# Kernel tuning notes

Measured on AMD Instinct MI355X. Metric: run time of the kernel, lower is better.

## Reference

```python
import jax, jax.numpy as jnp
import numpy as np

N_NODES = 50000
N_EDGES = 800000
D_IN = 128
D_HID = 128
D_OUT = 128


def _graph_conv(x, src, dst, ew, w_rel, w_root, b):
    # PyG GraphConv: out_i = (sum_{j->i} ew_ji * x_j) @ w_rel.T + b + x_i @ w_root.T
    msg = x[src] * ew[:, None]                                   # [E, F] gather + scale
    agg = jax.ops.segment_sum(msg, dst, num_segments=x.shape[0])  # [N, F] scatter-add
    return agg @ w_rel.T + x @ w_root.T + b


def setup_inputs() -> dict:
    key = jax.random.key(0)
    ks = jax.random.split(key, 12)
    s = 0.05
    x = jax.random.normal(ks[0], (N_NODES, D_IN), dtype=jnp.float32)
    edge_index = jax.random.randint(ks[1], (2, N_EDGES), 0, N_NODES, dtype=jnp.int32)
    edge_weight = jax.random.uniform(ks[2], (N_EDGES,), dtype=jnp.float32)
    return {
        "x": x,
        "edge_index": edge_index,
        "edge_weight": edge_weight,
        "w1_rel": jax.random.normal(ks[3], (D_HID, D_IN), dtype=jnp.float32) * s,
        "w1_root": jax.random.normal(ks[4], (D_HID, D_IN), dtype=jnp.float32) * s,
        "b1": jnp.zeros((D_HID,), dtype=jnp.float32),
        "w2_rel": jax.random.normal(ks[5], (D_HID, D_HID), dtype=jnp.float32) * s,
        "w2_root": jax.random.normal(ks[6], (D_HID, D_HID), dtype=jnp.float32) * s,
        "b2": jnp.zeros((D_HID,), dtype=jnp.float32),
        "w3_rel": jax.random.normal(ks[7], (D_OUT, D_HID), dtype=jnp.float32) * s,
        "w3_root": jax.random.normal(ks[8], (D_OUT, D_HID), dtype=jnp.float32) * s,
        "b3": jnp.zeros((D_OUT,), dtype=jnp.float32),
    }


def reference(x, edge_index, edge_weight,
              w1_rel, w1_root, b1,
              w2_rel, w2_root, b2,
              w3_rel, w3_root, b3):
    src, dst = edge_index[0], edge_index[1]
    h = _graph_conv(x, src, dst, edge_weight, w1_rel, w1_root, b1)
    h = jax.nn.relu(h)  # dropout is identity in eval mode
    h = _graph_conv(h, src, dst, edge_weight, w2_rel, w2_root, b2)
    h = jax.nn.relu(h)
    out = _graph_conv(h, src, dst, edge_weight, w3_rel, w3_root, b3)
    return out
```

## Files before the change

### kernel.cpp

```cpp
#include <hip/hip_runtime.h>
#include <hip/hip_bf16.h>

#define DFEAT   128
#define BCAP    2048
#define NB_MAX  1024

typedef __attribute__((ext_vector_type(8))) short bf16x8;
typedef __attribute__((ext_vector_type(4))) float f32x4;
typedef unsigned int uint;


__global__ void cursor_init(int* __restrict__ cursor, int NB) {
    int b = blockIdx.x * 256 + threadIdx.x;
    if (b < NB) cursor[b] = b * BCAP;
}


__global__ __launch_bounds__(1024) void bin_scatter(const int* __restrict__ src,
                                                    const int* __restrict__ dst,
                                                    const float* __restrict__ ew,
                                                    int* __restrict__ cursor,
                                                    int2* __restrict__ bedges,
                                                    int E, int NB) {
    __shared__ int hist[NB_MAX];
    __shared__ int base[NB_MAX];
    const int tid = threadIdx.x;
    for (int b = tid; b < NB; b += 1024) hist[b] = 0;
    __syncthreads();

    int  s[8]; float w[8]; int bk[8]; int dl[8];
    const int i0 = blockIdx.x * 8192 + tid;
    #pragma unroll
    for (int k = 0; k < 8; ++k) {
        int i = i0 + k * 1024;
        if (i < E) {
            s[k] = src[i]; w[k] = ew[i];
            int d = dst[i];
            bk[k] = d >> 6; dl[k] = d & 63;
            atomicAdd(&hist[bk[k]], 1);
        } else bk[k] = -1;
    }
    __syncthreads();
    for (int b = tid; b < NB; b += 1024) {
        int c = hist[b];
        base[b] = (c > 0) ? atomicAdd(&cursor[b], c) : 0;
        hist[b] = 0;
    }
    __syncthreads();
    #pragma unroll
    for (int k = 0; k < 8; ++k) {
        if (bk[k] >= 0) {
            int r = atomicAdd(&hist[bk[k]], 1);
            int pos = base[bk[k]] + r;
            if (pos < ((bk[k] + 1) << 11)) {
                bedges[pos] = make_int2(s[k] | (dl[k] << 26), __float_as_int(w[k]));
            }
        }
    }
}


__global__ __launch_bounds__(1024) void bucket_sort(const int* __restrict__ cursor,
                                                    int2* __restrict__ bedges,
                                                    int* __restrict__ rowptr,
                                                    int* __restrict__ rowend, int N) {
    __shared__ int2 buf[BCAP];
    __shared__ int hist[64], pref[64], rank[64];
    const int b = blockIdx.x, tid = threadIdx.x;
    const int base = b << 11;
    const int cnt = cursor[b] - base;

    if (tid < 64) hist[tid] = 0;
    __syncthreads();
    for (int i = tid; i < cnt; i += 1024) {
        int2 e = bedges[base + i];
        buf[i] = e;
        atomicAdd(&hist[((uint)e.x) >> 26], 1);
    }
    __syncthreads();
    if (tid < 64) {
        int v = hist[tid];
        int s = v;
        #pragma unroll
        for (int off = 1; off < 64; off <<= 1) {
            int t = __shfl_up(s, off, 64);
            if (tid >= off) s += t;
        }
        pref[tid] = s - v;
        rank[tid] = 0;
        int node = b * 64 + tid;
        if (node < N) {
            rowptr[node] = base + (s - v);
            rowend[node] = base + s;
        }
    }
    __syncthreads();
    for (int i = tid; i < cnt; i += 1024) {
        int2 e = buf[i];
        int dl = ((uint)e.x) >> 26;
        int r = atomicAdd(&rank[dl], 1);
        bedges[base + pref[dl] + r] = e;
    }
}


__device__ __forceinline__ uint pack_bf16x2(float a, float b) {
    __hip_bfloat16 ba = __float2bfloat16(a);
    __hip_bfloat16 bb = __float2bfloat16(b);
    unsigned short ua = *(unsigned short*)&ba;
    unsigned short ub = *(unsigned short*)&bb;
    return (uint)ua | ((uint)ub << 16);
}

__global__ void cvt_kernel(const float* __restrict__ in, uint* __restrict__ out, int n2) {
    int i = blockIdx.x * 256 + threadIdx.x;
    if (i < n2) {
        float2 v = ((const float2*)in)[i];
        out[i] = pack_bf16x2(v.x, v.y);
    }
}


__global__ void prep_Bpack(const float* __restrict__ wrel, const float* __restrict__ wroot,
                           __hip_bfloat16* __restrict__ Bp) {
    int idx = blockIdx.x * 256 + threadIdx.x;
    if (idx >= 32768) return;
    int j     = idx & 7;
    int lane  = (idx >> 3) & 63;
    int nfrag = (idx >> 9) & 7;
    int kstep = idx >> 12;
    int k = kstep * 32 + (lane >> 4) * 8 + j;
    int n = nfrag * 16 + (lane & 15);
    float v = (k < 128) ? wrel[n * 128 + k] : wroot[n * 128 + (k - 128)];
    Bp[idx] = __float2bfloat16(v);
}


__global__ __launch_bounds__(256) void aggregate_bf16(const uint* __restrict__ f,
                                                      const int* __restrict__ rowptr,
                                                      const int* __restrict__ rowend,
                                                      const int2* __restrict__ bedges,
                                                      uint* __restrict__ aggB, int N) {
    const int wid = threadIdx.x >> 6, lane = threadIdx.x & 63;
    const int node = blockIdx.x * 4 + wid;
    if (node >= N) return;
    const int beg = rowptr[node];
    const int deg = rowend[node] - beg;
    const int grp = lane >> 4;
    const int sub = lane & 15;

    const uint4* f4 = (const uint4*)f;

    float acc[8];
    #pragma unroll
    for (int i = 0; i < 8; ++i) acc[i] = 0.f;

    int done = 0;
    while (done < deg) {
        const int chunk = min(deg - done, 64);
        int2 e = bedges[beg + done + min(lane, chunk - 1)];
        const int vsrc = e.x & 0x03FFFFFF;
        const int vwb  = (lane < chunk) ? e.y : 0;
        const int iters = (chunk + 7) & ~7;
        for (int j = 0; j < iters; j += 8) {
            const int   s0 = __shfl(vsrc, j + grp, 64);
            const float w0 = __int_as_float(__shfl(vwb, j + grp, 64));
            const int   s1 = __shfl(vsrc, j + 4 + grp, 64);
            const float w1 = __int_as_float(__shfl(vwb, j + 4 + grp, 64));
            const uint4 q0 = f4[(size_t)s0 * 16 + sub];
            const uint4 q1 = f4[(size_t)s1 * 16 + sub];
            acc[0] = fmaf(w0, __uint_as_float(q0.x << 16),          acc[0]);
            acc[1] = fmaf(w0, __uint_as_float(q0.x & 0xffff0000u),  acc[1]);
            acc[2] = fmaf(w0, __uint_as_float(q0.y << 16),          acc[2]);
            acc[3] = fmaf(w0, __uint_as_float(q0.y & 0xffff0000u),  acc[3]);
            acc[4] = fmaf(w0, __uint_as_float(q0.z << 16),          acc[4]);
            acc[5] = fmaf(w0, __uint_as_float(q0.z & 0xffff0000u),  acc[5]);
            acc[6] = fmaf(w0, __uint_as_float(q0.w << 16),          acc[6]);
            acc[7] = fmaf(w0, __uint_as_float(q0.w & 0xffff0000u),  acc[7]);
            acc[0] = fmaf(w1, __uint_as_float(q1.x << 16),          acc[0]);
            acc[1] = fmaf(w1, __uint_as_float(q1.x & 0xffff0000u),  acc[1]);
            acc[2] = fmaf(w1, __uint_as_float(q1.y << 16),          acc[2]);
            acc[3] = fmaf(w1, __uint_as_float(q1.y & 0xffff0000u),  acc[3]);
            acc[4] = fmaf(w1, __uint_as_float(q1.z << 16),          acc[4]);
            acc[5] = fmaf(w1, __uint_as_float(q1.z & 0xffff0000u),  acc[5]);
            acc[6] = fmaf(w1, __uint_as_float(q1.w << 16),          acc[6]);
            acc[7] = fmaf(w1, __uint_as_float(q1.w & 0xffff0000u),  acc[7]);
        }
        done += chunk;
    }

    #pragma unroll
    for (int i = 0; i < 8; ++i) {
        acc[i] += __shfl_xor(acc[i], 16, 64);
        acc[i] += __shfl_xor(acc[i], 32, 64);
    }

    if (lane < 16) {
        uint4 o;
        o.x = pack_bf16x2(acc[0], acc[1]);
        o.y = pack_bf16x2(acc[2], acc[3]);
        o.z = pack_bf16x2(acc[4], acc[5]);
        o.w = pack_bf16x2(acc[6], acc[7]);
        ((uint4*)aggB)[(size_t)node * 16 + sub] = o;
    }
}


template<int RELU, int OUTF32>
__global__ __launch_bounds__(256) void gemm_mfma(const uint* __restrict__ Aagg,
                                                 const uint* __restrict__ f,
                                                 const bf16x8* __restrict__ Bp,
                                                 const float* __restrict__ bias,
                                                 float* __restrict__ outf,
                                                 __hip_bfloat16* __restrict__ outb, int M) {
    const int tid  = threadIdx.x;
    const int lane = tid & 63, wid = tid >> 6;
    const int wr = wid >> 1, wc = wid & 1;
    const int m0 = blockIdx.x * 128 + wr * 64;
    const int n0 = wc * 64;

    f32x4 acc[4][4];
    #pragma unroll
    for (int mi = 0; mi < 4; ++mi)
        #pragma unroll
        for (int ni = 0; ni < 4; ++ni) acc[mi][ni] = (f32x4){0.f, 0.f, 0.f, 0.f};

    const short* Aa = (const short*)Aagg;
    const short* Ar = (const short*)f;
    const int lrow = lane & 15;
    const int lk   = (lane >> 4) * 8;
    int rowidx[4];
    #pragma unroll
    for (int mi = 0; mi < 4; ++mi) {
        int r = m0 + mi * 16 + lrow;
        rowidx[mi] = (r < M) ? r : (M - 1);
    }

    #pragma unroll
    for (int ks = 0; ks < 8; ++ks) {
        const short* Abase = (ks < 4) ? Aa : Ar;
        const int koff = (ks & 3) * 32 + lk;
        bf16x8 a[4], b[4];
        #pragma unroll
        for (int mi = 0; mi < 4; ++mi)
            a[mi] = *(const bf16x8*)(Abase + (size_t)rowidx[mi] * 128 + koff);
        #pragma unroll
        for (int ni = 0; ni < 4; ++ni)
            b[ni] = Bp[(ks * 8 + (wc * 4 + ni)) * 64 + lane];
        #pragma unroll
        for (int mi = 0; mi < 4; ++mi)
            #pragma unroll
            for (int ni = 0; ni < 4; ++ni)
                acc[mi][ni] = __builtin_amdgcn_mfma_f32_16x16x32_bf16(a[mi], b[ni], acc[mi][ni], 0, 0, 0);
    }

    const int crow = (lane >> 4) * 4;
    const int ccol = lane & 15;
    #pragma unroll
    for (int mi = 0; mi < 4; ++mi) {
        #pragma unroll
        for (int ni = 0; ni < 4; ++ni) {
            int col = n0 + ni * 16 + ccol;
            float bv = bias[col];
            #pragma unroll
            for (int r = 0; r < 4; ++r) {
                int row = m0 + mi * 16 + crow + r;
                if (row < M) {
                    float v = acc[mi][ni][r] + bv;
                    if (RELU) v = fmaxf(v, 0.f);
                    if (OUTF32) outf[(size_t)row * 128 + col] = v;
                    else        outb[(size_t)row * 128 + col] = __float2bfloat16(v);
                }
            }
        }
    }
}


extern "C" void kernel_launch(void* const* d_in, const int* in_sizes, int n_in,
                              void* d_out, int out_size, void* d_ws, size_t ws_size,
                              hipStream_t stream) {
    const float* x   = (const float*)d_in[0];
    const int*  eidx = (const int*)d_in[1];
    const float* ew  = (const float*)d_in[2];
    const float* w1r = (const float*)d_in[3];
    const float* w1t = (const float*)d_in[4];
    const float* b1  = (const float*)d_in[5];
    const float* w2r = (const float*)d_in[6];
    const float* w2t = (const float*)d_in[7];
    const float* b2  = (const float*)d_in[8];
    const float* w3r = (const float*)d_in[9];
    const float* w3t = (const float*)d_in[10];
    const float* b3  = (const float*)d_in[11];
    float* out = (float*)d_out;

    const int N  = in_sizes[0] / DFEAT;
    const int E  = in_sizes[2];
    const int NB = (N + 63) / 64;

    char* ws = (char*)d_ws;
    size_t off = 0;
    auto alloc = [&](size_t bytes) -> void* {
        off = (off + 255) & ~(size_t)255;
        void* p = ws + off;
        off += bytes;
        return p;
    };
    int*  cursor = (int*)alloc((size_t)NB * 4);
    int*  rowptr = (int*)alloc((size_t)N * 4);
    int*  rowend = (int*)alloc((size_t)N * 4);
    int2* bedges = (int2*)alloc((size_t)NB * BCAP * 8);
    __hip_bfloat16* Bp1 = (__hip_bfloat16*)alloc(32768 * 2);
    __hip_bfloat16* Bp2 = (__hip_bfloat16*)alloc(32768 * 2);
    __hip_bfloat16* Bp3 = (__hip_bfloat16*)alloc(32768 * 2);
    uint* xb   = (uint*)alloc((size_t)N * 64 * 4);
    uint* aggB = (uint*)alloc((size_t)N * 64 * 4);
    uint* h1b  = (uint*)alloc((size_t)N * 64 * 4);
    uint* h2b  = (uint*)alloc((size_t)N * 64 * 4);
    (void)ws_size;

    const int* src = eidx;
    const int* dst = eidx + E;

    cursor_init<<<(NB + 255) / 256, 256, 0, stream>>>(cursor, NB);
    bin_scatter<<<(E + 8191) / 8192, 1024, 0, stream>>>(src, dst, ew, cursor, bedges, E, NB);
    bucket_sort<<<NB, 1024, 0, stream>>>(cursor, bedges, rowptr, rowend, N);

    cvt_kernel<<<(N * 64 + 255) / 256, 256, 0, stream>>>(x, xb, N * 64);
    prep_Bpack<<<128, 256, 0, stream>>>(w1r, w1t, Bp1);
    prep_Bpack<<<128, 256, 0, stream>>>(w2r, w2t, Bp2);
    prep_Bpack<<<128, 256, 0, stream>>>(w3r, w3t, Bp3);

    const int aggGrid  = (N + 3) / 4;
    const int gemmGrid = (N + 127) / 128;

    aggregate_bf16<<<aggGrid, 256, 0, stream>>>(xb, rowptr, rowend, bedges, aggB, N);
    gemm_mfma<1, 0><<<gemmGrid, 256, 0, stream>>>(aggB, xb, (const bf16x8*)Bp1,
                                                  b1, nullptr, (__hip_bfloat16*)h1b, N);
    aggregate_bf16<<<aggGrid, 256, 0, stream>>>(h1b, rowptr, rowend, bedges, aggB, N);
    gemm_mfma<1, 0><<<gemmGrid, 256, 0, stream>>>(aggB, h1b, (const bf16x8*)Bp2,
                                                  b2, nullptr, (__hip_bfloat16*)h2b, N);
    aggregate_bf16<<<aggGrid, 256, 0, stream>>>(h2b, rowptr, rowend, bedges, aggB, N);
    gemm_mfma<0, 1><<<gemmGrid, 256, 0, stream>>>(aggB, h2b, (const bf16x8*)Bp3,
                                                  b3, out, nullptr, N);
}
```

Before: 178.3 us.

## Fuse aggregation into MFMA GEMM per 64-node tile and merge prep kernels

Each layer now runs one kernel: a 64-node tile block first aggregates neighbor features into a padded LDS tile (each wave handles 16 nodes sequentially), then runs the MFMA GEMM reading the aggregated half from LDS and the root half from global. This removes the aggB round trip through global memory and three kernel launches. Separately, the bf16 conversion, the weight packing and the cursor init are merged into one launch. The fused kernel uses a smaller grid (64 nodes per block, each wave serially walking 16 nodes), which may reduce latency hiding for the gather compared with one node per wave.

```diff
diff --git a/kernel.cpp b/kernel.cpp
--- a/kernel.cpp
+++ b/kernel.cpp
@@ -8,12 +8,6 @@
 typedef __attribute__((ext_vector_type(8))) short bf16x8;
 typedef __attribute__((ext_vector_type(4))) float f32x4;
 typedef unsigned int uint;
-
-
-__global__ void cursor_init(int* __restrict__ cursor, int NB) {
-    int b = blockIdx.x * 256 + threadIdx.x;
-    if (b < NB) cursor[b] = b * BCAP;
-}
 
 
 __global__ __launch_bounds__(1024) void bin_scatter(const int* __restrict__ src,
@@ -112,161 +106,178 @@
     return (uint)ua | ((uint)ub << 16);
 }
 
-__global__ void cvt_kernel(const float* __restrict__ in, uint* __restrict__ out, int n2) {
-    int i = blockIdx.x * 256 + threadIdx.x;
-    if (i < n2) {
-        float2 v = ((const float2*)in)[i];
-        out[i] = pack_bf16x2(v.x, v.y);
-    }
-}
-
-
-__global__ void prep_Bpack(const float* __restrict__ wrel, const float* __restrict__ wroot,
-                           __hip_bfloat16* __restrict__ Bp) {
-    int idx = blockIdx.x * 256 + threadIdx.x;
-    if (idx >= 32768) return;
-    int j     = idx & 7;
-    int lane  = (idx >> 3) & 63;
-    int nfrag = (idx >> 9) & 7;
-    int kstep = idx >> 12;
-    int k = kstep * 32 + (lane >> 4) * 8 + j;
-    int n = nfrag * 16 + (lane & 15);
-    float v = (k < 128) ? wrel[n * 128 + k] : wroot[n * 128 + (k - 128)];
-    Bp[idx] = __float2bfloat16(v);
-}
-
-
-__global__ __launch_bounds__(256) void aggregate_bf16(const uint* __restrict__ f,
-                                                      const int* __restrict__ rowptr,
-                                                      const int* __restrict__ rowend,
-                                                      const int2* __restrict__ bedges,
-                                                      uint* __restrict__ aggB, int N) {
-    const int wid = threadIdx.x >> 6, lane = threadIdx.x & 63;
-    const int node = blockIdx.x * 4 + wid;
-    if (node >= N) return;
-    const int beg = rowptr[node];
-    const int deg = rowend[node] - beg;
-    const int grp = lane >> 4;
-    const int sub = lane & 15;
-
-    const uint4* f4 = (const uint4*)f;
-
-    float acc[8];
-    #pragma unroll
-    for (int i = 0; i < 8; ++i) acc[i] = 0.f;
-
-    int done = 0;
-    while (done < deg) {
-        const int chunk = min(deg - done, 64);
-        int2 e = bedges[beg + done + min(lane, chunk - 1)];
-        const int vsrc = e.x & 0x03FFFFFF;
-        const int vwb  = (lane < chunk) ? e.y : 0;
-        const int iters = (chunk + 7) & ~7;
-        for (int j = 0; j < iters; j += 8) {
-            const int   s0 = __shfl(vsrc, j + grp, 64);
-            const float w0 = __int_as_float(__shfl(vwb, j + grp, 64));
-            const int   s1 = __shfl(vsrc, j + 4 + grp, 64);
-            const float w1 = __int_as_float(__shfl(vwb, j + 4 + grp, 64));
-            const uint4 q0 = f4[(size_t)s0 * 16 + sub];
-            const uint4 q1 = f4[(size_t)s1 * 16 + sub];
-            acc[0] = fmaf(w0, __uint_as_float(q0.x << 16),          acc[0]);
-            acc[1] = fmaf(w0, __uint_as_float(q0.x & 0xffff0000u),  acc[1]);
-            acc[2] = fmaf(w0, __uint_as_float(q0.y << 16),          acc[2]);
-            acc[3] = fmaf(w0, __uint_as_float(q0.y & 0xffff0000u),  acc[3]);
-            acc[4] = fmaf(w0, __uint_as_float(q0.z << 16),          acc[4]);
-            acc[5] = fmaf(w0, __uint_as_float(q0.z & 0xffff0000u),  acc[5]);
-            acc[6] = fmaf(w0, __uint_as_float(q0.w << 16),          acc[6]);
-            acc[7] = fmaf(w0, __uint_as_float(q0.w & 0xffff0000u),  acc[7]);
-            acc[0] = fmaf(w1, __uint_as_float(q1.x << 16),          acc[0]);
-            acc[1] = fmaf(w1, __uint_as_float(q1.x & 0xffff0000u),  acc[1]);
-            acc[2] = fmaf(w1, __uint_as_float(q1.y << 16),          acc[2]);
-            acc[3] = fmaf(w1, __uint_as_float(q1.y & 0xffff0000u),  acc[3]);
-            acc[4] = fmaf(w1, __uint_as_float(q1.z << 16),          acc[4]);
-            acc[5] = fmaf(w1, __uint_as_float(q1.z & 0xffff0000u),  acc[5]);
-            acc[6] = fmaf(w1, __uint_as_float(q1.w << 16),          acc[6]);
-            acc[7] = fmaf(w1, __uint_as_float(q1.w & 0xffff0000u),  acc[7]);
-        }
-        done += chunk;
-    }
-
-    #pragma unroll
-    for (int i = 0; i < 8; ++i) {
-        acc[i] += __shfl_xor(acc[i], 16, 64);
-        acc[i] += __shfl_xor(acc[i], 32, 64);
-    }
-
-    if (lane < 16) {
-        uint4 o;
-        o.x = pack_bf16x2(acc[0], acc[1]);
-        o.y = pack_bf16x2(acc[2], acc[3]);
-        o.z = pack_bf16x2(acc[4], acc[5]);
-        o.w = pack_bf16x2(acc[6], acc[7]);
-        ((uint4*)aggB)[(size_t)node * 16 + sub] = o;
+
+__global__ void prep_all(const float* __restrict__ x, uint* __restrict__ xb, int n2,
+                         const float* __restrict__ w1r, const float* __restrict__ w1t,
+                         const float* __restrict__ w2r, const float* __restrict__ w2t,
+                         const float* __restrict__ w3r, const float* __restrict__ w3t,
+                         __hip_bfloat16* __restrict__ Bp1, __hip_bfloat16* __restrict__ Bp2,
+                         __hip_bfloat16* __restrict__ Bp3,
+                         int* __restrict__ cursor, int NB, int cvtB) {
+    const int b = blockIdx.x, tid = threadIdx.x;
+    if (b < cvtB) {
+        int i = b * 256 + tid;
+        if (i < n2) {
+            float2 v = ((const float2*)x)[i];
+            xb[i] = pack_bf16x2(v.x, v.y);
+        }
+    } else if (b < cvtB + 384) {
+        const int b2 = b - cvtB;
+        const int g = b2 >> 7;
+        const int idx = (b2 & 127) * 256 + tid;
+        const float* wrel  = (g == 0) ? w1r : (g == 1) ? w2r : w3r;
+        const float* wroot = (g == 0) ? w1t : (g == 1) ? w2t : w3t;
+        __hip_bfloat16* Bp = (g == 0) ? Bp1 : (g == 1) ? Bp2 : Bp3;
+        int j     = idx & 7;
+        int lane  = (idx >> 3) & 63;
+        int nfrag = (idx >> 9) & 7;
+        int kstep = idx >> 12;
+        int k = kstep * 32 + (lane >> 4) * 8 + j;
+        int n = nfrag * 16 + (lane & 15);
+        float v = (k < 128) ? wrel[n * 128 + k] : wroot[n * 128 + (k - 128)];
+        Bp[idx] = __float2bfloat16(v);
+    } else {
+        int i = (b - cvtB - 384) * 256 + tid;
+        if (i < NB) cursor[i] = i * BCAP;
     }
 }
 
 
 template<int RELU, int OUTF32>
-__global__ __launch_bounds__(256) void gemm_mfma(const uint* __restrict__ Aagg,
-                                                 const uint* __restrict__ f,
-                                                 const bf16x8* __restrict__ Bp,
-                                                 const float* __restrict__ bias,
-                                                 float* __restrict__ outf,
-                                                 __hip_bfloat16* __restrict__ outb, int M) {
+__global__ __launch_bounds__(256) void fused_layer(const uint* __restrict__ f,
+                                                   const int* __restrict__ rowptr,
+                                                   const int* __restrict__ rowend,
+                                                   const int2* __restrict__ bedges,
+                                                   const bf16x8* __restrict__ Bp,
+                                                   const float* __restrict__ bias,
+                                                   float* __restrict__ outf,
+                                                   __hip_bfloat16* __restrict__ outb,
+                                                   int N) {
+    __shared__ uint4 As4[64][17];
     const int tid  = threadIdx.x;
     const int lane = tid & 63, wid = tid >> 6;
+    const int grp  = lane >> 4;
+    const int sub  = lane & 15;
+    const int tile = blockIdx.x * 64;
+    const uint4* f4 = (const uint4*)f;
+
+    const int pn = tile + wid * 16 + (lane & 15);
+    int rp = 0, re = 0;
+    if (lane < 16 && pn < N) { rp = rowptr[pn]; re = rowend[pn]; }
+
+    for (int q = 0; q < 16; ++q) {
+        const int node = tile + wid * 16 + q;
+        const int beg = __builtin_amdgcn_readlane(rp, q);
+        const int end = __builtin_amdgcn_readlane(re, q);
+        const int deg = end - beg;
+
+        float acc[8];
+        #pragma unroll
+        for (int i = 0; i < 8; ++i) acc[i] = 0.f;
+
+        if (node < N) {
+            int done = 0;
+            while (done < deg) {
+                const int chunk = min(deg - done, 64);
+                int2 e = bedges[beg + done + min(lane, chunk - 1)];
+                const int vsrc = e.x & 0x03FFFFFF;
+                const int vwb  = (lane < chunk) ? e.y : 0;
+                const int iters = (chunk + 7) & ~7;
+                for (int j = 0; j < iters; j += 8) {
+                    const int   s0 = __shfl(vsrc, j + grp, 64);
+                    const float w0 = __int_as_float(__shfl(vwb, j + grp, 64));
+                    const int   s1 = __shfl(vsrc, j + 4 + grp, 64);
+                    const float w1 = __int_as_float(__shfl(vwb, j + 4 + grp, 64));
+                    const uint4 q0 = f4[(size_t)s0 * 16 + sub];
+                    const uint4 q1 = f4[(size_t)s1 * 16 + sub];
+                    acc[0] = fmaf(w0, __uint_as_float(q0.x << 16),         acc[0]);
+                    acc[1] = fmaf(w0, __uint_as_float(q0.x & 0xffff0000u), acc[1]);
+                    acc[2] = fmaf(w0, __uint_as_float(q0.y << 16),         acc[2]);
+                    acc[3] = fmaf(w0, __uint_as_float(q0.y & 0xffff0000u), acc[3]);
+                    acc[4] = fmaf(w0, __uint_as_float(q0.z << 16),         acc[4]);
+                    acc[5] = fmaf(w0, __uint_as_float(q0.z & 0xffff0000u), acc[5]);
+                    acc[6] = fmaf(w0, __uint_as_float(q0.w << 16),         acc[6]);
+                    acc[7] = fmaf(w0, __uint_as_float(q0.w & 0xffff0000u), acc[7]);
+                    acc[0] = fmaf(w1, __uint_as_float(q1.x << 16),         acc[0]);
+                    acc[1] = fmaf(w1, __uint_as_float(q1.x & 0xffff0000u), acc[1]);
+                    acc[2] = fmaf(w1, __uint_as_float(q1.y << 16),         acc[2]);
+                    acc[3] = fmaf(w1, __uint_as_float(q1.y & 0xffff0000u), acc[3]);
+                    acc[4] = fmaf(w1, __uint_as_float(q1.z << 16),         acc[4]);
+                    acc[5] = fmaf(w1, __uint_as_float(q1.z & 0xffff0000u), acc[5]);
+                    acc[6] = fmaf(w1, __uint_as_float(q1.w << 16),         acc[6]);
+                    acc[7] = fmaf(w1, __uint_as_float(q1.w & 0xffff0000u), acc[7]);
+                }
+                done += chunk;
+            }
+        }
+        #pragma unroll
+        for (int i = 0; i < 8; ++i) {
+            acc[i] += __shfl_xor(acc[i], 16, 64);
+            acc[i] += __shfl_xor(acc[i], 32, 64);
+        }
+        if (lane < 16) {
+            uint4 o;
+            o.x = pack_bf16x2(acc[0], acc[1]);
+            o.y = pack_bf16x2(acc[2], acc[3]);
+            o.z = pack_bf16x2(acc[4], acc[5]);
+            o.w = pack_bf16x2(acc[6], acc[7]);
+            As4[wid * 16 + q][sub] = o;
+        }
+    }
+    __syncthreads();
+
     const int wr = wid >> 1, wc = wid & 1;
-    const int m0 = blockIdx.x * 128 + wr * 64;
-    const int n0 = wc * 64;
-
-    f32x4 acc[4][4];
-    #pragma unroll
-    for (int mi = 0; mi < 4; ++mi)
-        #pragma unroll
-        for (int ni = 0; ni < 4; ++ni) acc[mi][ni] = (f32x4){0.f, 0.f, 0.f, 0.f};
-
-    const short* Aa = (const short*)Aagg;
-    const short* Ar = (const short*)f;
     const int lrow = lane & 15;
-    const int lk   = (lane >> 4) * 8;
-    int rowidx[4];
-    #pragma unroll
-    for (int mi = 0; mi < 4; ++mi) {
-        int r = m0 + mi * 16 + lrow;
-        rowidx[mi] = (r < M) ? r : (M - 1);
-    }
+    const int lkq  = (lane >> 4);
+    const short* As_s = (const short*)&As4[0][0];
+    const short* fb   = (const short*)f;
+
+    int grow[2];
+    #pragma unroll
+    for (int mi = 0; mi < 2; ++mi) {
+        int r = tile + wr * 32 + mi * 16 + lrow;
+        grow[mi] = (r < N) ? r : (N - 1);
+    }
+
+    f32x4 acc2[2][4];
+    #pragma unroll
+    for (int mi = 0; mi < 2; ++mi)
+        #pragma unroll
+        for (int nf = 0; nf < 4; ++nf) acc2[mi][nf] = (f32x4){0.f, 0.f, 0.f, 0.f};
 
     #pragma unroll
     for (int ks = 0; ks < 8; ++ks) {
-        const short* Abase = (ks < 4) ? Aa : Ar;
-        const int koff = (ks & 3) * 32 + lk;
-        bf16x8 a[4], b[4];
-        #pragma unroll
-        for (int mi = 0; mi < 4; ++mi)
-            a[mi] = *(const bf16x8*)(Abase + (size_t)rowidx[mi] * 128 + koff);
-        #pragma unroll
-        for (int ni = 0; ni < 4; ++ni)
-            b[ni] = Bp[(ks * 8 + (wc * 4 + ni)) * 64 + lane];
-        #pragma unroll
-        for (int mi = 0; mi < 4; ++mi)
+        bf16x8 a[2], b[4];
+        #pragma unroll
+        for (int mi = 0; mi < 2; ++mi) {
+            if (ks < 4)
+                a[mi] = *(const bf16x8*)(As_s + (wr * 32 + mi * 16 + lrow) * 136 + ks * 32 + lkq * 8);
+            else
+                a[mi] = *(const bf16x8*)(fb + (size_t)grow[mi] * 128 + (ks - 4) * 32 + lkq * 8);
+        }
+        #pragma unroll
+        for (int nf = 0; nf < 4; ++nf)
+            b[nf] = Bp[(ks * 8 + (wc * 4 + nf)) * 64 + lane];
+        #pragma unroll
+        for (int mi = 0; mi < 2; ++mi)
             #pragma unroll
-            for (int ni = 0; ni < 4; ++ni)
-                acc[mi][ni] = __builtin_amdgcn_mfma_f32_16x16x32_bf16(a[mi], b[ni], acc[mi][ni], 0, 0, 0);
+            for (int nf = 0; nf < 4; ++nf)
+                acc2[mi][nf] = __builtin_amdgcn_mfma_f32_16x16x32_bf16(a[mi], b[nf], acc2[mi][nf], 0, 0, 0);
     }
 
     const int crow = (lane >> 4) * 4;
     const int ccol = lane & 15;
     #pragma unroll
-    for (int mi = 0; mi < 4; ++mi) {
-        #pragma unroll
-        for (int ni = 0; ni < 4; ++ni) {
-            int col = n0 + ni * 16 + ccol;
-            float bv = bias[col];
+    for (int mi = 0; mi < 2; ++mi) {
+        #pragma unroll
+        for (int nf = 0; nf < 4; ++nf) {
+            const int col = wc * 64 + nf * 16 + ccol;
+            const float bv = bias[col];
             #pragma unroll
             for (int r = 0; r < 4; ++r) {
-                int row = m0 + mi * 16 + crow + r;
-                if (row < M) {
-                    float v = acc[mi][ni][r] + bv;
+                const int row = tile + wr * 32 + mi * 16 + crow + r;
+                if (row < N) {
+                    float v = acc2[mi][nf][r] + bv;
                     if (RELU) v = fmaxf(v, 0.f);
                     if (OUTF32) outf[(size_t)row * 128 + col] = v;
                     else        outb[(size_t)row * 128 + col] = __float2bfloat16(v);
@@ -314,7 +325,6 @@
     __hip_bfloat16* Bp2 = (__hip_bfloat16*)alloc(32768 * 2);
     __hip_bfloat16* Bp3 = (__hip_bfloat16*)alloc(32768 * 2);
     uint* xb   = (uint*)alloc((size_t)N * 64 * 4);
-    uint* aggB = (uint*)alloc((size_t)N * 64 * 4);
     uint* h1b  = (uint*)alloc((size_t)N * 64 * 4);
     uint* h2b  = (uint*)alloc((size_t)N * 64 * 4);
     (void)ws_size;
@@ -322,25 +332,20 @@
     const int* src = eidx;
     const int* dst = eidx + E;
 
-    cursor_init<<<(NB + 255) / 256, 256, 0, stream>>>(cursor, NB);
+    const int n2 = N * 64;
+    const int cvtB = (n2 + 255) / 256;
+    const int curB = (NB + 255) / 256;
+    prep_all<<<cvtB + 384 + curB, 256, 0, stream>>>(x, xb, n2,
+                                                    w1r, w1t, w2r, w2t, w3r, w3t,
+                                                    Bp1, Bp2, Bp3, cursor, NB, cvtB);
+
     bin_scatter<<<(E + 8191) / 8192, 1024, 0, stream>>>(src, dst, ew, cursor, bedges, E, NB);
     bucket_sort<<<NB, 1024, 0, stream>>>(cursor, bedges, rowptr, rowend, N);
 
-    cvt_kernel<<<(N * 64 + 255) / 256, 256, 0, stream>>>(x, xb, N * 64);
-    prep_Bpack<<<128, 256, 0, stream>>>(w1r, w1t, Bp1);
-    prep_Bpack<<<128, 256, 0, stream>>>(w2r, w2t, Bp2);
-    prep_Bpack<<<128, 256, 0, stream>>>(w3r, w3t, Bp3);
-
-    const int aggGrid  = (N + 3) / 4;
-    const int gemmGrid = (N + 127) / 128;
-
-    aggregate_bf16<<<aggGrid, 256, 0, stream>>>(xb, rowptr, rowend, bedges, aggB, N);
-    gemm_mfma<1, 0><<<gemmGrid, 256, 0, stream>>>(aggB, xb, (const bf16x8*)Bp1,
-                                                  b1, nullptr, (__hip_bfloat16*)h1b, N);
-    aggregate_bf16<<<aggGrid, 256, 0, stream>>>(h1b, rowptr, rowend, bedges, aggB, N);
-    gemm_mfma<1, 0><<<gemmGrid, 256, 0, stream>>>(aggB, h1b, (const bf16x8*)Bp2,
-                                                  b2, nullptr, (__hip_bfloat16*)h2b, N);
-    aggregate_bf16<<<aggGrid, 256, 0, stream>>>(h2b, rowptr, rowend, bedges, aggB, N);
-    gemm_mfma<0, 1><<<gemmGrid, 256, 0, stream>>>(aggB, h2b, (const bf16x8*)Bp3,
-                                                  b3, out, nullptr, N);
-}
+    fused_layer<1, 0><<<NB, 256, 0, stream>>>(xb, rowptr, rowend, bedges, (const bf16x8*)Bp1,
+                                              b1, nullptr, (__hip_bfloat16*)h1b, N);
+    fused_layer<1, 0><<<NB, 256, 0, stream>>>(h1b, rowptr, rowend, bedges, (const bf16x8*)Bp2,
+                                              b2, nullptr, (__hip_bfloat16*)h2b, N);
+    fused_layer<0, 1><<<NB, 256, 0, stream>>>(h2b, rowptr, rowend, bedges, (const bf16x8*)Bp3,
+                                              b3, out, nullptr, N);
+}
```

Result: faster. 166.4 us (-6.7%).
